# Kernel optimization log

Hardware: AMD Instinct MI355X
Metric: run time of the kernel (lower is better)

Reference implementation:

```python
import jax, jax.numpy as jnp
import numpy as np
import math

B, S, D, H = 4, 2048, 1024, 16
HD = D // H  # head_dim = 64


def setup_inputs() -> dict:
    key = jax.random.key(0)
    ks = jax.random.split(key, 5)
    x = jax.random.normal(ks[0], (B, S, D), dtype=jnp.float32)
    # causal mask, broadcastable over batch and heads
    mask = jnp.tril(jnp.ones((S, S), dtype=bool))[None, None]
    # Linear params in [in, out] layout (math-equivalent to torch's [out, in])
    w_attn = jax.random.normal(ks[1], (D, 3 * D), dtype=jnp.float32) * (1.0 / math.sqrt(D))
    b_attn = jax.random.normal(ks[2], (3 * D,), dtype=jnp.float32) * 0.02
    w_proj = jax.random.normal(ks[3], (D, D), dtype=jnp.float32) * (1.0 / math.sqrt(D))
    b_proj = jax.random.normal(ks[4], (D,), dtype=jnp.float32) * 0.02
    return {"x": x, "mask": mask, "w_attn": w_attn, "b_attn": b_attn,
            "w_proj": w_proj, "b_proj": b_proj}


def reference(x, mask, w_attn, b_attn, w_proj, b_proj):
    b, s, d = x.shape
    # fused qkv projection, then split heads -> [b, h, s, hd]
    qkv = x @ w_attn + b_attn
    q, k, v = jnp.split(qkv, 3, axis=-1)
    split = lambda t: t.reshape(b, s, H, HD).transpose(0, 2, 1, 3)
    q, k, v = split(q), split(k), split(v)
    # scaled dot-product attention with boolean mask (True = keep)
    scores = jnp.einsum('bhqd,bhkd->bhqk', q, k) / math.sqrt(HD)
    scores = jnp.where(mask, scores, -jnp.inf)
    attn = jax.nn.softmax(scores, axis=-1)  # attn_dropout with p=0 is identity
    out = jnp.einsum('bhqk,bhkd->bhqd', attn, v)
    out = out.transpose(0, 2, 1, 3).reshape(b, s, d)
    # output projection (resid_dropout with p=0 is identity)
    return out @ w_proj + b_proj
```

## Files before the change

kernel.cpp:

```cpp
#include <hip/hip_runtime.h>

typedef unsigned short u16;
typedef __attribute__((ext_vector_type(4))) float floatx4;
typedef __attribute__((ext_vector_type(8))) short shortx8;

#define B_ 4
#define S_ 2048
#define D_ 1024
#define H_ 16
#define HD_ 64

__device__ __forceinline__ float b2f(u16 u) {
    return __uint_as_float(((unsigned int)u) << 16);
}
__device__ __forceinline__ u16 f2b(float f) {
    unsigned int u = __float_as_uint(f);
    u += 0x7fffu + ((u >> 16) & 1u);
    return (u16)(u >> 16);
}
__device__ __forceinline__ unsigned long long pack4(float a, float b, float c, float d) {
    return (unsigned long long)f2b(a) | ((unsigned long long)f2b(b) << 16) |
           ((unsigned long long)f2b(c) << 32) | ((unsigned long long)f2b(d) << 48);
}
__device__ __forceinline__ unsigned int permpk(float a, float b) {
    return __builtin_amdgcn_perm(__float_as_uint(b) + 0x8000u,
                                 __float_as_uint(a) + 0x8000u, 0x07060302u);
}
__device__ __forceinline__ void glds16(const u16* g, u16* l) {
    __builtin_amdgcn_global_load_lds(
        (const __attribute__((address_space(1))) unsigned int*)g,
        (__attribute__((address_space(3))) unsigned int*)l, 16, 0, 0);
}
__device__ __forceinline__ void bar() {
    asm volatile("" ::: "memory");
    __builtin_amdgcn_s_barrier();
    asm volatile("" ::: "memory");
}
#define VMW4 asm volatile("s_waitcnt vmcnt(4)" ::: "memory")
#define VMW2 asm volatile("s_waitcnt vmcnt(2)" ::: "memory")
#define VMW0 asm volatile("s_waitcnt vmcnt(0)" ::: "memory")

__global__ void detect_dtype(const unsigned int* __restrict__ x, int* __restrict__ flag) {
    const int l = threadIdx.x;
    int cnt = 0;
    for (int i = l; i < 4096; i += 64) {
        const unsigned int e = (x[i] >> 7) & 0xffu;
        cnt += (e >= 110u && e <= 134u) ? 1 : 0;
    }
#pragma unroll
    for (int d = 1; d < 64; d <<= 1) cnt += __shfl_xor(cnt, d);
    if (l == 0) *flag = (cnt > 2048) ? 1 : 0;
}

__global__ __launch_bounds__(256) void convert_x(const void* __restrict__ xin,
                                                 u16* __restrict__ xb,
                                                 const void* __restrict__ bA,
                                                 const void* __restrict__ bP,
                                                 u16* __restrict__ bAb,
                                                 u16* __restrict__ bPb,
                                                 const int* __restrict__ flag) {
    const int isbf = *flag;
    const size_t i = ((size_t)blockIdx.x * 256 + threadIdx.x) * 8;
    if (isbf) {
        *(uint4*)(xb + i) = *(const uint4*)((const u16*)xin + i);
    } else {
        const float* xf = (const float*)xin;
        float4 a = *(const float4*)(xf + i);
        float4 b = *(const float4*)(xf + i + 4);
        u16 o[8] = {f2b(a.x), f2b(a.y), f2b(a.z), f2b(a.w),
                    f2b(b.x), f2b(b.y), f2b(b.z), f2b(b.w)};
        *(uint4*)(xb + i) = *(uint4*)o;
    }
    if (blockIdx.x == 0) {
        for (int j = threadIdx.x; j < 3072; j += 256)
            bAb[j] = isbf ? ((const u16*)bA)[j] : f2b(((const float*)bA)[j]);
        for (int j = threadIdx.x; j < 1024; j += 256)
            bPb[j] = isbf ? ((const u16*)bP)[j] : f2b(((const float*)bP)[j]);
    }
}

__global__ __launch_bounds__(256) void transpose_both(const void* __restrict__ inA,
                                                      u16* __restrict__ outA,
                                                      const void* __restrict__ inP,
                                                      u16* __restrict__ outP,
                                                      const int* __restrict__ flag) {
    const int isbf = *flag;
    __shared__ u16 tile[32][33];
    const int tx = threadIdx.x & 31;
    const int ty = threadIdx.x >> 5;
    int bxi = blockIdx.x;
    const void* in;
    u16* out;
    int N;
    if (bxi < 96) { in = inA; out = outA; N = 3072; }
    else          { in = inP; out = outP; N = 1024; bxi -= 96; }
    const int K = 1024;
    const int bx = bxi * 32;
    const int by = blockIdx.y * 32;
    if (isbf) {
#pragma unroll
        for (int i = 0; i < 32; i += 8)
            tile[ty + i][tx] = ((const u16*)in)[(size_t)(by + ty + i) * N + bx + tx];
    } else {
#pragma unroll
        for (int i = 0; i < 32; i += 8)
            tile[ty + i][tx] = f2b(((const float*)in)[(size_t)(by + ty + i) * N + bx + tx]);
    }
    __syncthreads();
#pragma unroll
    for (int i = 0; i < 32; i += 8)
        out[(size_t)(bx + ty + i) * K + by + tx] = tile[tx][ty + i];
}

template <int MODE>
__global__ __launch_bounds__(256) void gemm_bt(const u16* __restrict__ A,
                                               const u16* __restrict__ BT,
                                               const u16* __restrict__ bias,
                                               void* __restrict__ outv,
                                               int M, int N, int K,
                                               u16* __restrict__ qws,
                                               u16* __restrict__ kws,
                                               u16* __restrict__ vws,
                                               const int* __restrict__ flag) {
    __shared__ __align__(16) u16 As[3][128 * 32];
    __shared__ __align__(16) u16 Bs[3][128 * 32];

    const int isbf = (MODE == 0) ? *flag : 1;
    const int tid = threadIdx.x;
    const int w = tid >> 6, l = tid & 63;
    const int lane_m = l & 15, quad = l >> 4;
    const int bm = blockIdx.x * 128, bn = blockIdx.y * 128;
    const int wm = (w >> 1) * 64, wn = (w & 1) * 64;

    floatx4 acc[4][4];
#pragma unroll
    for (int i = 0; i < 4; i++)
#pragma unroll
        for (int j = 0; j < 4; j++) acc[i][j] = (floatx4){0.f, 0.f, 0.f, 0.f};

    const int lr = l >> 2, sl = l & 3;
    const int cA = sl ^ ((lr >> 1) & 3);
    const int rb0 = w * 16, rb1 = 64 + w * 16;
    const u16* Arow0 = A + (size_t)(bm + rb0 + lr) * K + cA * 8;
    const u16* Arow1 = A + (size_t)(bm + rb1 + lr) * K + cA * 8;
    const u16* Brow0 = BT + (size_t)(bn + rb0 + lr) * K + cA * 8;
    const u16* Brow1 = BT + (size_t)(bn + rb1 + lr) * K + cA * 8;

    auto stage = [&](int t) {
        const int k0 = t * 32;
        u16* ad = &As[t % 3][0];
        u16* bd = &Bs[t % 3][0];
        glds16(Arow0 + k0, ad + rb0 * 32);
        glds16(Arow1 + k0, ad + rb1 * 32);
        glds16(Brow0 + k0, bd + rb0 * 32);
        glds16(Brow1 + k0, bd + rb1 * 32);
    };

    const int NT = K >> 5;
    stage(0);
    stage(1);
    for (int t = 0; t < NT; ++t) {
        if (t < NT - 1) { VMW4; } else { VMW0; }
        bar();
        if (t + 2 < NT) stage(t + 2);

        const u16* Ac = &As[t % 3][0];
        const u16* Bc = &Bs[t % 3][0];
        shortx8 af[4], bf[4];
#pragma unroll
        for (int mb = 0; mb < 4; mb++) {
            const int r = wm + mb * 16 + lane_m;
            af[mb] = *(const shortx8*)(Ac + r * 32 + (quad ^ ((r >> 1) & 3)) * 8);
        }
#pragma unroll
        for (int nb = 0; nb < 4; nb++) {
            const int r = wn + nb * 16 + lane_m;
            bf[nb] = *(const shortx8*)(Bc + r * 32 + (quad ^ ((r >> 1) & 3)) * 8);
        }
#pragma unroll
        for (int mb = 0; mb < 4; mb++)
#pragma unroll
            for (int nb = 0; nb < 4; nb++)
                acc[mb][nb] = __builtin_amdgcn_mfma_f32_16x16x32_bf16(
                    af[mb], bf[nb], acc[mb][nb], 0, 0, 0);
    }

    const float SCALE_Q = 0.18033688011112042f;

    if (MODE == 1 && (bn >> 10) == 2) {
        __syncthreads();
        u16* ep = (w < 2) ? &As[w][0] : &Bs[w - 2][0];
#pragma unroll
        for (int nb = 0; nb < 4; nb++) {
            const int lhd = nb * 16 + lane_m;
            const float bv = b2f(bias[bn + wn + lhd]);
            const int sw = (lhd & 7) << 3;
#pragma unroll
            for (int mb = 0; mb < 4; mb++) {
                const int o = mb * 16 + quad * 4;
                unsigned long long pk =
                    pack4(acc[mb][nb][0] + bv, acc[mb][nb][1] + bv,
                          acc[mb][nb][2] + bv, acc[mb][nb][3] + bv);
                *(unsigned long long*)(ep + lhd * 64 + (o ^ sw)) = pk;
            }
        }
        __syncthreads();
        const int bI = bm >> 11;
        const int hI = ((bn + wn) >> 6) & 15;
        const int s0 = (bm & 2047) + wm;
        u16* vb0 = vws + (size_t)(bI * 16 + hI) * 64 * 2048;
        const int rr8 = l >> 3, c8 = l & 7;
#pragma unroll
        for (int p = 0; p < 8; p++) {
            const int lhd = p * 8 + rr8;
            uint4 v4 = *(const uint4*)(ep + lhd * 64 + ((c8 << 3) ^ ((lhd & 7) << 3)));
            *(uint4*)(vb0 + (size_t)lhd * 2048 + s0 + c8 * 8) = v4;
        }
    } else {
#pragma unroll
        for (int nb = 0; nb < 4; nb++) {
            const int col = bn + wn + nb * 16 + lane_m;
            const float bv = b2f(bias[col]);
#pragma unroll
            for (int mb = 0; mb < 4; mb++) {
                const int rowb = bm + wm + mb * 16 + quad * 4;
#pragma unroll
                for (int r = 0; r < 4; r++) {
                    float v = acc[mb][nb][r] + bv;
                    const int rr = rowb + r;
                    if (MODE == 0) {
                        if (isbf) ((u16*)outv)[(size_t)rr * N + col] = f2b(v);
                        else ((float*)outv)[(size_t)rr * N + col] = v;
                    } else {
                        const int which = col >> 10;
                        if (which == 0) v *= SCALE_Q;
                        const int h = (col >> 6) & 15;
                        const int hd = col & 63;
                        const int b = rr >> 11, s = rr & 2047;
                        u16* dst = which == 0 ? qws : kws;
                        dst[((size_t)(b * 16 + h) * 2048 + s) * 64 + hd] = f2b(v);
                    }
                }
            }
        }
    }
}

__global__ __launch_bounds__(512, 4) void attn_kernel(const u16* __restrict__ Qg,
                                                      const u16* __restrict__ Kg,
                                                      const u16* __restrict__ Vtg,
                                                      u16* __restrict__ Og) {
    __shared__ __align__(16) u16 Ks[3][64 * 64];
    __shared__ __align__(16) u16 Vs[3][64 * 64];
    __shared__ __align__(16) u16 Ps[8][16 * 72];

    const int tid = threadIdx.x, w = tid >> 6, l = tid & 63;
    const int lane_m = l & 15, quad = l >> 4;
    const int bh = blockIdx.y;
    const u16* qp = Qg + (size_t)bh * S_ * 64;
    const u16* kp = Kg + (size_t)bh * S_ * 64;
    const u16* vtp = Vtg + (size_t)bh * 64 * S_;
    u16* psw = &Ps[w][0];
    const int b = bh >> 4, h = bh & 15;

    const int lr8 = l >> 3, sl8 = l & 7;
    const int cK = sl8 ^ (lr8 & 7);
    const int rbase = w * 8;
    const u16* Kr = kp + (size_t)(rbase + lr8) * 64 + cK * 8;
    const u16* Vr = vtp + (size_t)(rbase + lr8) * S_ + cK * 8;

    auto stage = [&](int t) {
        const int k0 = t * 64;
        glds16(Kr + (size_t)k0 * 64, &Ks[t % 3][0] + rbase * 64);
        glds16(Vr + k0, &Vs[t % 3][0] + rbase * 64);
    };

    for (int pass = 0; pass < 2; pass++) {
        const int xm = pass ? (15 - (int)blockIdx.x) : (int)blockIdx.x;
        const int q0 = xm * 128;
        const int qw0 = q0 + w * 16;

        shortx8 qF[2];
#pragma unroll
        for (int ks = 0; ks < 2; ks++)
            qF[ks] = *(const shortx8*)(qp + (size_t)(qw0 + lane_m) * 64 + ks * 32 + quad * 8);

        floatx4 o_acc[4];
#pragma unroll
        for (int md = 0; md < 4; md++) o_acc[md] = (floatx4){0.f, 0.f, 0.f, 0.f};
        float m_i = -1e30f, l_i = 0.f;

        const int ntiles = (q0 >> 6) + 2;
        const int myend = qw0 + 15;

        __syncthreads();
        stage(0);
        stage(1);
        for (int t = 0; t < ntiles; t++) {
            const int k0 = t * 64;
            if (t < ntiles - 1) { VMW2; } else { VMW0; }
            bar();
            if (t + 2 < ntiles) stage(t + 2);

            if (k0 <= myend) {
                const u16* kb = &Ks[t % 3][0];
                const u16* vb = &Vs[t % 3][0];
                floatx4 sc[4];
#pragma unroll
                for (int mb = 0; mb < 4; mb++) sc[mb] = (floatx4){0.f, 0.f, 0.f, 0.f};
#pragma unroll
                for (int ks = 0; ks < 2; ks++) {
                    shortx8 kA[4];
#pragma unroll
                    for (int mb = 0; mb < 4; mb++) {
                        const int r = mb * 16 + lane_m;
                        kA[mb] = *(const shortx8*)(kb + r * 64 + (((ks * 4 + quad) ^ (r & 7)) * 8));
                    }
                    __builtin_amdgcn_s_setprio(1);
#pragma unroll
                    for (int mb = 0; mb < 4; mb++)
                        sc[mb] = __builtin_amdgcn_mfma_f32_16x16x32_bf16(
                            kA[mb], qF[ks], sc[mb], 0, 0, 0);
                    __builtin_amdgcn_s_setprio(0);
                }

                const int qg = qw0 + lane_m;
                if (k0 + 63 > qw0) {
#pragma unroll
                    for (int mb = 0; mb < 4; mb++)
#pragma unroll
                        for (int r = 0; r < 4; r++) {
                            const int kvg = k0 + mb * 16 + quad * 4 + r;
                            if (kvg > qg) sc[mb][r] = -1e30f;
                        }
                }
                float mloc = -1e30f;
#pragma unroll
                for (int mb = 0; mb < 4; mb++) {
                    float a = fmaxf(fmaxf(sc[mb][0], sc[mb][1]),
                                    fmaxf(sc[mb][2], sc[mb][3]));
                    mloc = fmaxf(mloc, a);
                }
                mloc = fmaxf(mloc, __shfl_xor(mloc, 16));
                mloc = fmaxf(mloc, __shfl_xor(mloc, 32));
                float mnew = m_i;
                if (!__all(mloc <= m_i + 8.0f)) {
                    mnew = fmaxf(m_i, mloc);
                    const float alpha = __builtin_amdgcn_exp2f(m_i - mnew);
                    m_i = mnew;
                    l_i *= alpha;
#pragma unroll
                    for (int md = 0; md < 4; md++) o_acc[md] *= alpha;
                }
                float psum = 0.f;
#pragma unroll
                for (int mb = 0; mb < 4; mb++) {
                    const float p0 = __builtin_amdgcn_exp2f(sc[mb][0] - mnew);
                    const float p1 = __builtin_amdgcn_exp2f(sc[mb][1] - mnew);
                    const float p2 = __builtin_amdgcn_exp2f(sc[mb][2] - mnew);
                    const float p3 = __builtin_amdgcn_exp2f(sc[mb][3] - mnew);
                    psum += (p0 + p1) + (p2 + p3);
                    uint2 pk = {permpk(p0, p1), permpk(p2, p3)};
                    *(uint2*)(psw + lane_m * 72 + mb * 16 + quad * 4) = pk;
                }
                psum += __shfl_xor(psum, 16);
                psum += __shfl_xor(psum, 32);
                l_i += psum;

#pragma unroll
                for (int ks = 0; ks < 2; ks++) {
                    shortx8 vF[4], pF;
#pragma unroll
                    for (int md = 0; md < 4; md++) {
                        const int r = md * 16 + lane_m;
                        vF[md] = *(const shortx8*)(vb + r * 64 + (((ks * 4 + quad) ^ (r & 7)) * 8));
                    }
                    pF = *(const shortx8*)(psw + lane_m * 72 + ks * 32 + quad * 8);
                    __builtin_amdgcn_s_setprio(1);
#pragma unroll
                    for (int md = 0; md < 4; md++)
                        o_acc[md] = __builtin_amdgcn_mfma_f32_16x16x32_bf16(
                            vF[md], pF, o_acc[md], 0, 0, 0);
                    __builtin_amdgcn_s_setprio(0);
                }
            }
        }

        {
            const float inv = 1.0f / l_i;
            const int qg = qw0 + lane_m;
            const size_t base = ((size_t)b * 2048 + qg) * 1024 + h * 64;
#pragma unroll
            for (int md = 0; md < 4; md++) {
                *(unsigned long long*)(Og + base + md * 16 + quad * 4) =
                    pack4(o_acc[md][0] * inv, o_acc[md][1] * inv,
                          o_acc[md][2] * inv, o_acc[md][3] * inv);
            }
        }
    }
}

extern "C" void kernel_launch(void* const* d_in, const int* in_sizes, int n_in,
                              void* d_out, int out_size, void* d_ws, size_t ws_size,
                              hipStream_t stream) {
    const void* x      = d_in[0];
    const void* w_attn = d_in[2];
    const void* b_attn = d_in[3];
    const void* w_proj = d_in[4];
    const void* b_proj = d_in[5];

    u16* qws = (u16*)d_ws;
    u16* kws = qws + 8388608;
    u16* vws = kws + 8388608;
    u16* xb  = vws + 8388608;
    u16* aws = xb;
    u16* wtA = xb + 8388608;
    u16* wtP = wtA + 3145728;
    u16* bAb = wtP + 1048576;
    u16* bPb = bAb + 3072;
    int* flag = (int*)(bPb + 1024);

    detect_dtype<<<1, 64, 0, stream>>>((const unsigned int*)x, flag);
    convert_x<<<4096, 256, 0, stream>>>(x, xb, b_attn, b_proj, bAb, bPb, flag);
    transpose_both<<<dim3(128, 32), 256, 0, stream>>>(w_attn, wtA, w_proj, wtP, flag);

    gemm_bt<1><<<dim3(8192 / 128, 3072 / 128), 256, 0, stream>>>(
        xb, wtA, bAb, nullptr, 8192, 3072, 1024, qws, kws, vws, flag);

    attn_kernel<<<dim3(8, B_ * H_), 512, 0, stream>>>(qws, kws, vws, aws);

    gemm_bt<0><<<dim3(8192 / 128, 1024 / 128), 256, 0, stream>>>(
        aws, wtP, bPb, d_out, 8192, 1024, 1024, nullptr, nullptr, nullptr, flag);
}
```

Measured before the change: 296.6 us.

## Fuse preprocessing kernels and switch attention K/V staging to double buffering

Merges dtype detection, x/bias conversion and weight transposition into one preproc kernel, so two launches and the global flag dependency go away. Each block now detects the dtype itself from 256 words of x. The attention kernel goes from a three-slot K/V ring with prefetch distance two and explicit vmcnt waits to a two-slot ring with prefetch distance one and plain __syncthreads. That cuts LDS use per block, but it shortens the load-ahead window and may expose global-load latency in the dominant attention loop.

```diff
diff --git a/kernel.cpp b/kernel.cpp
--- a/kernel.cpp
+++ b/kernel.cpp
@@ -37,79 +37,79 @@
     asm volatile("" ::: "memory");
 }
 #define VMW4 asm volatile("s_waitcnt vmcnt(4)" ::: "memory")
-#define VMW2 asm volatile("s_waitcnt vmcnt(2)" ::: "memory")
 #define VMW0 asm volatile("s_waitcnt vmcnt(0)" ::: "memory")
 
-__global__ void detect_dtype(const unsigned int* __restrict__ x, int* __restrict__ flag) {
-    const int l = threadIdx.x;
-    int cnt = 0;
-    for (int i = l; i < 4096; i += 64) {
-        const unsigned int e = (x[i] >> 7) & 0xffu;
-        cnt += (e >= 110u && e <= 134u) ? 1 : 0;
-    }
-#pragma unroll
-    for (int d = 1; d < 64; d <<= 1) cnt += __shfl_xor(cnt, d);
-    if (l == 0) *flag = (cnt > 2048) ? 1 : 0;
-}
-
-__global__ __launch_bounds__(256) void convert_x(const void* __restrict__ xin,
-                                                 u16* __restrict__ xb,
-                                                 const void* __restrict__ bA,
-                                                 const void* __restrict__ bP,
-                                                 u16* __restrict__ bAb,
-                                                 u16* __restrict__ bPb,
-                                                 const int* __restrict__ flag) {
-    const int isbf = *flag;
-    const size_t i = ((size_t)blockIdx.x * 256 + threadIdx.x) * 8;
-    if (isbf) {
-        *(uint4*)(xb + i) = *(const uint4*)((const u16*)xin + i);
-    } else {
-        const float* xf = (const float*)xin;
-        float4 a = *(const float4*)(xf + i);
-        float4 b = *(const float4*)(xf + i + 4);
-        u16 o[8] = {f2b(a.x), f2b(a.y), f2b(a.z), f2b(a.w),
-                    f2b(b.x), f2b(b.y), f2b(b.z), f2b(b.w)};
-        *(uint4*)(xb + i) = *(uint4*)o;
-    }
-    if (blockIdx.x == 0) {
-        for (int j = threadIdx.x; j < 3072; j += 256)
-            bAb[j] = isbf ? ((const u16*)bA)[j] : f2b(((const float*)bA)[j]);
-        for (int j = threadIdx.x; j < 1024; j += 256)
-            bPb[j] = isbf ? ((const u16*)bP)[j] : f2b(((const float*)bP)[j]);
-    }
-}
-
-__global__ __launch_bounds__(256) void transpose_both(const void* __restrict__ inA,
-                                                      u16* __restrict__ outA,
-                                                      const void* __restrict__ inP,
-                                                      u16* __restrict__ outP,
-                                                      const int* __restrict__ flag) {
-    const int isbf = *flag;
+__global__ __launch_bounds__(256) void preproc(const void* __restrict__ xin,
+                                               u16* __restrict__ xb,
+                                               const void* __restrict__ bA,
+                                               const void* __restrict__ bP,
+                                               u16* __restrict__ bAb,
+                                               u16* __restrict__ bPb,
+                                               const void* __restrict__ wA,
+                                               u16* __restrict__ wtA,
+                                               const void* __restrict__ wP,
+                                               u16* __restrict__ wtP,
+                                               int* __restrict__ flag) {
+    __shared__ int cnts[4];
     __shared__ u16 tile[32][33];
-    const int tx = threadIdx.x & 31;
-    const int ty = threadIdx.x >> 5;
-    int bxi = blockIdx.x;
-    const void* in;
-    u16* out;
-    int N;
-    if (bxi < 96) { in = inA; out = outA; N = 3072; }
-    else          { in = inP; out = outP; N = 1024; bxi -= 96; }
-    const int K = 1024;
-    const int bx = bxi * 32;
-    const int by = blockIdx.y * 32;
-    if (isbf) {
-#pragma unroll
-        for (int i = 0; i < 32; i += 8)
-            tile[ty + i][tx] = ((const u16*)in)[(size_t)(by + ty + i) * N + bx + tx];
-    } else {
-#pragma unroll
-        for (int i = 0; i < 32; i += 8)
-            tile[ty + i][tx] = f2b(((const float*)in)[(size_t)(by + ty + i) * N + bx + tx]);
+    const int tid = threadIdx.x;
+    {
+        const unsigned int e = (((const unsigned int*)xin)[tid] >> 7) & 0xffu;
+        int c = (e >= 110u && e <= 134u) ? 1 : 0;
+#pragma unroll
+        for (int d = 1; d < 64; d <<= 1) c += __shfl_xor(c, d);
+        if ((tid & 63) == 0) cnts[tid >> 6] = c;
     }
     __syncthreads();
-#pragma unroll
-    for (int i = 0; i < 32; i += 8)
-        out[(size_t)(bx + ty + i) * K + by + tx] = tile[tx][ty + i];
+    const int isbf = (cnts[0] + cnts[1] + cnts[2] + cnts[3] > 128) ? 1 : 0;
+
+    const int bid = blockIdx.x;
+    if (bid < 4096) {
+        const size_t i = ((size_t)bid * 256 + tid) * 8;
+        if (isbf) {
+            *(uint4*)(xb + i) = *(const uint4*)((const u16*)xin + i);
+        } else {
+            const float* xf = (const float*)xin;
+            float4 a = *(const float4*)(xf + i);
+            float4 b = *(const float4*)(xf + i + 4);
+            u16 o[8] = {f2b(a.x), f2b(a.y), f2b(a.z), f2b(a.w),
+                        f2b(b.x), f2b(b.y), f2b(b.z), f2b(b.w)};
+            *(uint4*)(xb + i) = *(uint4*)o;
+        }
+        if (bid == 0) {
+            if (tid == 0) *flag = isbf;
+            for (int j = tid; j < 3072; j += 256)
+                bAb[j] = isbf ? ((const u16*)bA)[j] : f2b(((const float*)bA)[j]);
+            for (int j = tid; j < 1024; j += 256)
+                bPb[j] = isbf ? ((const u16*)bP)[j] : f2b(((const float*)bP)[j]);
+        }
+    } else {
+        const int idx = bid - 4096;
+        int bxi = idx & 127;
+        const int by = (idx >> 7) * 32;
+        const void* in;
+        u16* out;
+        int N;
+        if (bxi < 96) { in = wA; out = wtA; N = 3072; }
+        else          { in = wP; out = wtP; N = 1024; bxi -= 96; }
+        const int K = 1024;
+        const int bx = bxi * 32;
+        const int tx = tid & 31;
+        const int ty = tid >> 5;
+        if (isbf) {
+#pragma unroll
+            for (int i = 0; i < 32; i += 8)
+                tile[ty + i][tx] = ((const u16*)in)[(size_t)(by + ty + i) * N + bx + tx];
+        } else {
+#pragma unroll
+            for (int i = 0; i < 32; i += 8)
+                tile[ty + i][tx] = f2b(((const float*)in)[(size_t)(by + ty + i) * N + bx + tx]);
+        }
+        __syncthreads();
+#pragma unroll
+        for (int i = 0; i < 32; i += 8)
+            out[(size_t)(bx + ty + i) * K + by + tx] = tile[tx][ty + i];
+    }
 }
 
 template <int MODE>
@@ -250,8 +250,8 @@
                                                       const u16* __restrict__ Kg,
                                                       const u16* __restrict__ Vtg,
                                                       u16* __restrict__ Og) {
-    __shared__ __align__(16) u16 Ks[3][64 * 64];
-    __shared__ __align__(16) u16 Vs[3][64 * 64];
+    __shared__ __align__(16) u16 Ks[2][64 * 64];
+    __shared__ __align__(16) u16 Vs[2][64 * 64];
     __shared__ __align__(16) u16 Ps[8][16 * 72];
 
     const int tid = threadIdx.x, w = tid >> 6, l = tid & 63;
@@ -271,8 +271,8 @@
 
     auto stage = [&](int t) {
         const int k0 = t * 64;
-        glds16(Kr + (size_t)k0 * 64, &Ks[t % 3][0] + rbase * 64);
-        glds16(Vr + k0, &Vs[t % 3][0] + rbase * 64);
+        glds16(Kr + (size_t)k0 * 64, &Ks[t & 1][0] + rbase * 64);
+        glds16(Vr + k0, &Vs[t & 1][0] + rbase * 64);
     };
 
     for (int pass = 0; pass < 2; pass++) {
@@ -295,16 +295,14 @@
 
         __syncthreads();
         stage(0);
-        stage(1);
         for (int t = 0; t < ntiles; t++) {
             const int k0 = t * 64;
-            if (t < ntiles - 1) { VMW2; } else { VMW0; }
-            bar();
-            if (t + 2 < ntiles) stage(t + 2);
+            __syncthreads();
+            if (t + 1 < ntiles) stage(t + 1);
 
             if (k0 <= myend) {
-                const u16* kb = &Ks[t % 3][0];
-                const u16* vb = &Vs[t % 3][0];
+                const u16* kb = &Ks[t & 1][0];
+                const u16* vb = &Vs[t & 1][0];
                 floatx4 sc[4];
 #pragma unroll
                 for (int mb = 0; mb < 4; mb++) sc[mb] = (floatx4){0.f, 0.f, 0.f, 0.f};
@@ -420,9 +418,8 @@
     u16* bPb = bAb + 3072;
     int* flag = (int*)(bPb + 1024);
 
-    detect_dtype<<<1, 64, 0, stream>>>((const unsigned int*)x, flag);
-    convert_x<<<4096, 256, 0, stream>>>(x, xb, b_attn, b_proj, bAb, bPb, flag);
-    transpose_both<<<dim3(128, 32), 256, 0, stream>>>(w_attn, wtA, w_proj, wtP, flag);
+    preproc<<<8192, 256, 0, stream>>>(x, xb, b_attn, b_proj, bAb, bPb,
+                                      w_attn, wtA, w_proj, wtP, flag);
 
     gemm_bt<1><<<dim3(8192 / 128, 3072 / 128), 256, 0, stream>>>(
         xb, wtA, bAb, nullptr, 8192, 3072, 1024, qws, kws, vws, flag);
```

Measured after the change: 280.3 us. -5.5%, faster.
